# Kernel tuning notes

Hardware: AMD Instinct MI355X
Metric: run time of the kernel (lower is better)

The kernel has to match this reference:

```python
import jax, jax.numpy as jnp
import numpy as np

B, L, D = 16, 96, 512
TAU = 1.0
SLOPE = 0.1  # LeakyReLU negative slope


def setup_inputs() -> dict:
    key = jax.random.key(0)
    k = jax.random.split(key, 6)
    inputs = jax.random.normal(k[0], (B, L, D), dtype=jnp.float32)
    mask = jnp.ones((B, L), dtype=jnp.int32)  # full-length samples
    order = jax.random.randint(k[1], (B, L), 0, L, dtype=jnp.int32)
    # torch Linear default init: U(-1/sqrt(fan_in), 1/sqrt(fan_in))
    s1 = 1.0 / np.sqrt(2 * D)
    s2 = 1.0 / np.sqrt(D)
    W1 = jax.random.uniform(k[2], (2 * D, D), jnp.float32, -s1, s1)
    b1 = jax.random.uniform(k[3], (D,), jnp.float32, -s1, s1)
    W2 = jax.random.uniform(k[4], (D, 1), jnp.float32, -s2, s2)
    b2 = jax.random.uniform(k[5], (1,), jnp.float32, -s2, s2)
    return {"inputs": inputs, "W1": W1, "b1": b1, "W2": W2, "b2": b2,
            "mask": mask, "order": order}


def reference(inputs, W1, b1, W2, b2, mask, order):
    # mask is all-ones -> every sample has length L, so the per-sample
    # slicing in the original is a no-op and we vectorize over the batch.
    # coh[b,i,j] = MLP(concat(x_i, x_j)); split W1 to avoid materializing
    # the [B, L*L, 2D] concatenated feature tensor.
    a = jnp.einsum('bld,dh->blh', inputs, W1[:D])   # contribution of x_i
    c = jnp.einsum('bld,dh->blh', inputs, W1[D:])   # contribution of x_j
    h = a[:, :, None, :] + c[:, None, :, :] + b1    # [B, L, L, D]
    h = jnp.where(h >= 0, h, SLOPE * h)             # LeakyReLU(0.1)
    coh = jnp.einsum('bijh,ho->bij', h, W2) + b2[0]  # [B, L, L]
    logits = coh / TAU

    # gt[b,i,j] = 1 iff order[b,i] - order[b,j] == -1 (j is i's successor)
    diff = order[:, :, None] - order[:, None, :]
    gt = (diff == -1).astype(jnp.int32)
    targets = jnp.argmax(gt, axis=-1).astype(jnp.int32)  # first max, like torch
    last = jnp.argmax(order, axis=-1)                     # last element has no successor
    targets = targets.at[jnp.arange(B), last].set(-1)     # ignore_index

    logp = jax.nn.log_softmax(logits, axis=-1)            # [B, L, L]
    safe_t = jnp.clip(targets, 0)
    picked = jnp.take_along_axis(logp, safe_t[..., None], axis=-1)[..., 0]
    valid = (targets != -1)
    # F.cross_entropy(reduction='mean', ignore_index=-1): mean over valid rows
    per_sample = (jnp.sum(jnp.where(valid, -picked, 0.0), axis=-1)
                  / jnp.sum(valid, axis=-1).astype(logp.dtype))
    return jnp.mean(per_sample)  # sum over samples / B
```

## Files before the change

kernel.cpp:

```cpp
#include <hip/hip_runtime.h>

#define BB 16
#define LL 96
#define DD 512
#define AC_ELEMS (1536 * 512)
#define LOGIT_ELEMS (BB * LL * LL)

__global__ __launch_bounds__(256) void gemm_ac(const float* __restrict__ X,
                                               const float* __restrict__ W1,
                                               const float* __restrict__ b1,
                                               float* __restrict__ a_ws,
                                               float* __restrict__ c_ws) {
  __shared__ float XsT[32][68];
  __shared__ float Ws[32][64];

  const int t = threadIdx.x;
  const int m0 = blockIdx.x * 64;
  const int part = blockIdx.y >> 3;
  const int n0 = (blockIdx.y & 7) * 64;
  const float* __restrict__ Wb = W1 + (size_t)part * (512 * 512);

  float acc[4][4] = {};

  const int r0 = (t >> 4) << 2;
  const int c0 = (t & 15) << 2;
  const int xrow = t >> 3;
  const int xcol = (t & 7) << 2;
  const int wkr = t >> 4;
  const int wc = (t & 15) << 2;

  for (int k0 = 0; k0 < 512; k0 += 32) {
    const float4 xv0 = *(const float4*)(X + (size_t)(m0 + xrow) * 512 + k0 + xcol);
    const float4 xv1 = *(const float4*)(X + (size_t)(m0 + xrow + 32) * 512 + k0 + xcol);
    const float4 wv0 = *(const float4*)(Wb + (size_t)(k0 + wkr) * 512 + n0 + wc);
    const float4 wv1 = *(const float4*)(Wb + (size_t)(k0 + wkr + 16) * 512 + n0 + wc);
    __syncthreads();
    XsT[xcol + 0][xrow] = xv0.x;
    XsT[xcol + 1][xrow] = xv0.y;
    XsT[xcol + 2][xrow] = xv0.z;
    XsT[xcol + 3][xrow] = xv0.w;
    XsT[xcol + 0][xrow + 32] = xv1.x;
    XsT[xcol + 1][xrow + 32] = xv1.y;
    XsT[xcol + 2][xrow + 32] = xv1.z;
    XsT[xcol + 3][xrow + 32] = xv1.w;
    *(float4*)&Ws[wkr][wc] = wv0;
    *(float4*)&Ws[wkr + 16][wc] = wv1;
    __syncthreads();

#pragma unroll
    for (int kk = 0; kk < 32; ++kk) {
      const float4 av = *(const float4*)&XsT[kk][r0];
      const float4 bv = *(const float4*)&Ws[kk][c0];
      acc[0][0] = fmaf(av.x, bv.x, acc[0][0]);
      acc[0][1] = fmaf(av.x, bv.y, acc[0][1]);
      acc[0][2] = fmaf(av.x, bv.z, acc[0][2]);
      acc[0][3] = fmaf(av.x, bv.w, acc[0][3]);
      acc[1][0] = fmaf(av.y, bv.x, acc[1][0]);
      acc[1][1] = fmaf(av.y, bv.y, acc[1][1]);
      acc[1][2] = fmaf(av.y, bv.z, acc[1][2]);
      acc[1][3] = fmaf(av.y, bv.w, acc[1][3]);
      acc[2][0] = fmaf(av.z, bv.x, acc[2][0]);
      acc[2][1] = fmaf(av.z, bv.y, acc[2][1]);
      acc[2][2] = fmaf(av.z, bv.z, acc[2][2]);
      acc[2][3] = fmaf(av.z, bv.w, acc[2][3]);
      acc[3][0] = fmaf(av.w, bv.x, acc[3][0]);
      acc[3][1] = fmaf(av.w, bv.y, acc[3][1]);
      acc[3][2] = fmaf(av.w, bv.z, acc[3][2]);
      acc[3][3] = fmaf(av.w, bv.w, acc[3][3]);
    }
  }

  float* __restrict__ outp = (part == 0) ? a_ws : c_ws;
  float4 bias;
  if (part == 0)
    bias = *(const float4*)(b1 + n0 + c0);
  else
    bias = make_float4(0.f, 0.f, 0.f, 0.f);
#pragma unroll
  for (int ri = 0; ri < 4; ++ri) {
    float4 v;
    v.x = acc[ri][0] + bias.x;
    v.y = acc[ri][1] + bias.y;
    v.z = acc[ri][2] + bias.z;
    v.w = acc[ri][3] + bias.w;
    *(float4*)(outp + (size_t)(m0 + r0 + ri) * 512 + n0 + c0) = v;
  }
}

__global__ __launch_bounds__(256) void coh_kernel(const float* __restrict__ a_ws,
                                                  const float* __restrict__ c_ws,
                                                  const float* __restrict__ W2,
                                                  float* __restrict__ logits) {
  __shared__ float As[16][516];
  __shared__ float Cs[16][516];
  __shared__ float w2s[512];

  const int b = blockIdx.x;
  const int it = blockIdx.y;
  const int jt = blockIdx.z;
  const int t = threadIdx.x;

  const float* __restrict__ abase = a_ws + ((size_t)b * 96 + it * 16) * 512;
  const float* __restrict__ cbase = c_ws + ((size_t)b * 96 + jt * 16) * 512;

#pragma unroll
  for (int p = 0; p < 8; ++p) {
    const int idx = p * 256 + t;
    const int row = idx >> 7;
    const int col = (idx & 127) << 2;
    *(float4*)&As[row][col] = *(const float4*)(abase + (size_t)row * 512 + col);
    *(float4*)&Cs[row][col] = *(const float4*)(cbase + (size_t)row * 512 + col);
  }
  if (t < 128) *(float4*)&w2s[t << 2] = *(const float4*)(W2 + (t << 2));
  __syncthreads();

  const int il = t >> 4;
  const int jl = t & 15;
  float acc = 0.f;
#pragma unroll 8
  for (int h = 0; h < 512; h += 4) {
    const float4 av = *(const float4*)&As[il][h];
    const float4 cv = *(const float4*)&Cs[jl][h];
    const float4 wv = *(const float4*)&w2s[h];
    float x;
    x = av.x + cv.x; acc = fmaf(fmaxf(x, 0.1f * x), wv.x, acc);
    x = av.y + cv.y; acc = fmaf(fmaxf(x, 0.1f * x), wv.y, acc);
    x = av.z + cv.z; acc = fmaf(fmaxf(x, 0.1f * x), wv.z, acc);
    x = av.w + cv.w; acc = fmaf(fmaxf(x, 0.1f * x), wv.w, acc);
  }
  logits[((size_t)b * 96 + it * 16 + il) * 96 + jt * 16 + jl] = acc;
}

__global__ __launch_bounds__(256) void loss_kernel(const float* __restrict__ logits,
                                                   const int* __restrict__ order,
                                                   float* __restrict__ out) {
  __shared__ float wsum[4];
  const int b = blockIdx.x / 6;
  const int rg = (blockIdx.x % 6) * 16;
  const int t = threadIdx.x;
  const int w = t >> 6;
  const int lane = t & 63;

  const int* __restrict__ ob = order + b * 96;
  const int ov = ob[lane];
  const int ov2 = (lane < 32) ? ob[64 + lane] : (int)0x80000000;

  int mo = (ov > ov2) ? ov : ov2;
#pragma unroll
  for (int d = 1; d < 64; d <<= 1) {
    const int o = __shfl_xor(mo, d);
    mo = (o > mo) ? o : mo;
  }
  const unsigned long long lm1 = __ballot(ov == mo);
  const unsigned long long lm2 = __ballot(lane < 32 && ov2 == mo);
  const int last = lm1 ? (__ffsll(lm1) - 1) : (64 + __ffsll(lm2) - 1);

  float lsum = 0.f;
  for (int r = rg + w; r < rg + 16; r += 4) {
    const float* __restrict__ lr = logits + ((size_t)b * 96 + r) * 96;
    const float l1 = lr[lane];
    const float l2 = (lane < 32) ? lr[64 + lane] : -1e30f;
    float m = fmaxf(l1, l2);
#pragma unroll
    for (int d = 1; d < 64; d <<= 1) m = fmaxf(m, __shfl_xor(m, d));
    float s = __expf(l1 - m) + ((lane < 32) ? __expf(l2 - m) : 0.f);
#pragma unroll
    for (int d = 1; d < 64; d <<= 1) s += __shfl_xor(s, d);
    const float lse = m + __logf(s);

    if (r != last) {
      const int oi = ob[r];
      const unsigned long long c1 = __ballot(ov == oi + 1);
      const unsigned long long c2 = __ballot(lane < 32 && ov2 == oi + 1);
      const int tj = c1 ? (__ffsll(c1) - 1) : (c2 ? (64 + __ffsll(c2) - 1) : 0);
      lsum += lse - lr[tj];
    }
  }
  if (lane == 0) wsum[w] = lsum;
  __syncthreads();
  if (t == 0) {
    atomicAdd(out, (wsum[0] + wsum[1] + wsum[2] + wsum[3]) * (1.0f / (16.0f * 95.0f)));
  }
}

extern "C" void kernel_launch(void* const* d_in, const int* in_sizes, int n_in,
                              void* d_out, int out_size, void* d_ws, size_t ws_size,
                              hipStream_t stream) {
  const float* X = (const float*)d_in[0];
  const float* W1 = (const float*)d_in[1];
  const float* b1 = (const float*)d_in[2];
  const float* W2 = (const float*)d_in[3];
  const int* order = (const int*)d_in[6];
  float* out = (float*)d_out;

  float* ws = (float*)d_ws;
  float* a_ws = ws;
  float* c_ws = ws + AC_ELEMS;
  float* logits = ws + 2 * AC_ELEMS;

  hipMemsetAsync(out, 0, sizeof(float), stream);
  gemm_ac<<<dim3(24, 16), 256, 0, stream>>>(X, W1, b1, a_ws, c_ws);
  coh_kernel<<<dim3(16, 6, 6), 256, 0, stream>>>(a_ws, c_ws, W2, logits);
  loss_kernel<<<96, 256, 0, stream>>>(logits, order, out);
}
```

Measured before the change: 121.7 us.

## Use bf16 MFMA for projection GEMM and register-tile the pairwise MLP kernel

Adds a prep kernel that converts X to bf16 and transposes W1 to bf16, then computes the two projection GEMMs with 16x16x32 bf16 MFMA instructions instead of fp32 FMA. The pairwise LeakyReLU/W2 kernel now computes a 2x2 output tile per thread over H chunks staged through shared memory, which cuts LDS traffic per output. This lowers the precision of the GEMM inputs and adds an extra launch plus conversion traffic on every call.

```diff
diff --git a/kernel.cpp b/kernel.cpp
--- a/kernel.cpp
+++ b/kernel.cpp
@@ -3,132 +3,182 @@
 #define BB 16
 #define LL 96
 #define DD 512
-#define AC_ELEMS (1536 * 512)
-#define LOGIT_ELEMS (BB * LL * LL)
-
-__global__ __launch_bounds__(256) void gemm_ac(const float* __restrict__ X,
-                                               const float* __restrict__ W1,
-                                               const float* __restrict__ b1,
-                                               float* __restrict__ a_ws,
-                                               float* __restrict__ c_ws) {
-  __shared__ float XsT[32][68];
-  __shared__ float Ws[32][64];
-
-  const int t = threadIdx.x;
-  const int m0 = blockIdx.x * 64;
-  const int part = blockIdx.y >> 3;
-  const int n0 = (blockIdx.y & 7) * 64;
-  const float* __restrict__ Wb = W1 + (size_t)part * (512 * 512);
-
-  float acc[4][4] = {};
-
-  const int r0 = (t >> 4) << 2;
-  const int c0 = (t & 15) << 2;
-  const int xrow = t >> 3;
-  const int xcol = (t & 7) << 2;
-  const int wkr = t >> 4;
-  const int wc = (t & 15) << 2;
+
+typedef short bf16x8 __attribute__((ext_vector_type(8)));
+typedef float f32x4 __attribute__((ext_vector_type(4)));
+typedef unsigned short us4 __attribute__((ext_vector_type(4)));
+
+static __device__ __forceinline__ unsigned short f2b(float f) {
+  union { float f; unsigned int u; } v; v.f = f;
+  unsigned int r = (v.u + 0x7FFFu + ((v.u >> 16) & 1u)) >> 16;
+  return (unsigned short)r;
+}
+
+__global__ __launch_bounds__(256) void prep(const float* __restrict__ X,
+                                            const float* __restrict__ W1,
+                                            unsigned short* __restrict__ xb,
+                                            unsigned short* __restrict__ w1t) {
+  const int t = threadIdx.x;
+  if (blockIdx.x < 768) {
+    const int g = blockIdx.x * 256 + t;
+    const float4 v = *(const float4*)(X + (size_t)g * 4);
+    us4 o;
+    o[0] = f2b(v.x); o[1] = f2b(v.y); o[2] = f2b(v.z); o[3] = f2b(v.w);
+    *(us4*)(xb + (size_t)g * 4) = o;
+  } else {
+    __shared__ float T[32][36];
+    const int tid = blockIdx.x - 768;
+    const int hb = tid & 15;
+    const int db = tid >> 4;
+    const int r = t >> 3;
+    const int c = (t & 7) * 4;
+    const float4 v = *(const float4*)(W1 + (size_t)(db * 32 + r) * 512 + hb * 32 + c);
+    T[r][c] = v.x; T[r][c + 1] = v.y; T[r][c + 2] = v.z; T[r][c + 3] = v.w;
+    __syncthreads();
+    us4 o;
+    o[0] = f2b(T[c + 0][r]); o[1] = f2b(T[c + 1][r]);
+    o[2] = f2b(T[c + 2][r]); o[3] = f2b(T[c + 3][r]);
+    const size_t idx = (size_t)(db >> 4) * (512 * 512) +
+                       (size_t)(hb * 32 + r) * 512 + (db & 15) * 32 + c;
+    *(us4*)(w1t + idx) = o;
+  }
+}
+
+__global__ __launch_bounds__(128) void gemm_mfma(const unsigned short* __restrict__ xb,
+                                                 const unsigned short* __restrict__ w1t,
+                                                 const float* __restrict__ bvec,
+                                                 float* __restrict__ a_ws,
+                                                 float* __restrict__ c_ws) {
+  __shared__ short Asm[32][40];
+  __shared__ short Bsm[64][40];
+  const int t = threadIdx.x;
+  const int m0 = blockIdx.x * 32;
+  const int n0 = blockIdx.y * 64;
+  const int part = blockIdx.z;
+  const unsigned short* __restrict__ Bg = w1t + (size_t)part * (512 * 512);
+  const int lane = t & 63;
+  const int w = t >> 6;
+
+  f32x4 acc[2][2] = {};
+
+  const int ar = t >> 2;
+  const int akq = (t & 3) << 3;
+  const int fr = lane & 15;
+  const int fg = lane >> 4;
 
   for (int k0 = 0; k0 < 512; k0 += 32) {
-    const float4 xv0 = *(const float4*)(X + (size_t)(m0 + xrow) * 512 + k0 + xcol);
-    const float4 xv1 = *(const float4*)(X + (size_t)(m0 + xrow + 32) * 512 + k0 + xcol);
-    const float4 wv0 = *(const float4*)(Wb + (size_t)(k0 + wkr) * 512 + n0 + wc);
-    const float4 wv1 = *(const float4*)(Wb + (size_t)(k0 + wkr + 16) * 512 + n0 + wc);
-    __syncthreads();
-    XsT[xcol + 0][xrow] = xv0.x;
-    XsT[xcol + 1][xrow] = xv0.y;
-    XsT[xcol + 2][xrow] = xv0.z;
-    XsT[xcol + 3][xrow] = xv0.w;
-    XsT[xcol + 0][xrow + 32] = xv1.x;
-    XsT[xcol + 1][xrow + 32] = xv1.y;
-    XsT[xcol + 2][xrow + 32] = xv1.z;
-    XsT[xcol + 3][xrow + 32] = xv1.w;
-    *(float4*)&Ws[wkr][wc] = wv0;
-    *(float4*)&Ws[wkr + 16][wc] = wv1;
-    __syncthreads();
-
-#pragma unroll
-    for (int kk = 0; kk < 32; ++kk) {
-      const float4 av = *(const float4*)&XsT[kk][r0];
-      const float4 bv = *(const float4*)&Ws[kk][c0];
-      acc[0][0] = fmaf(av.x, bv.x, acc[0][0]);
-      acc[0][1] = fmaf(av.x, bv.y, acc[0][1]);
-      acc[0][2] = fmaf(av.x, bv.z, acc[0][2]);
-      acc[0][3] = fmaf(av.x, bv.w, acc[0][3]);
-      acc[1][0] = fmaf(av.y, bv.x, acc[1][0]);
-      acc[1][1] = fmaf(av.y, bv.y, acc[1][1]);
-      acc[1][2] = fmaf(av.y, bv.z, acc[1][2]);
-      acc[1][3] = fmaf(av.y, bv.w, acc[1][3]);
-      acc[2][0] = fmaf(av.z, bv.x, acc[2][0]);
-      acc[2][1] = fmaf(av.z, bv.y, acc[2][1]);
-      acc[2][2] = fmaf(av.z, bv.z, acc[2][2]);
-      acc[2][3] = fmaf(av.z, bv.w, acc[2][3]);
-      acc[3][0] = fmaf(av.w, bv.x, acc[3][0]);
-      acc[3][1] = fmaf(av.w, bv.y, acc[3][1]);
-      acc[3][2] = fmaf(av.w, bv.z, acc[3][2]);
-      acc[3][3] = fmaf(av.w, bv.w, acc[3][3]);
-    }
+    const bf16x8 aval = *(const bf16x8*)(xb + (size_t)(m0 + ar) * 512 + k0 + akq);
+    const int i2 = t + 128;
+    const bf16x8 bv0 = *(const bf16x8*)(Bg + (size_t)(n0 + (t >> 2)) * 512 + k0 + ((t & 3) << 3));
+    const bf16x8 bv1 = *(const bf16x8*)(Bg + (size_t)(n0 + (i2 >> 2)) * 512 + k0 + ((i2 & 3) << 3));
+    __syncthreads();
+    *(bf16x8*)&Asm[ar][akq] = aval;
+    *(bf16x8*)&Bsm[t >> 2][(t & 3) << 3] = bv0;
+    *(bf16x8*)&Bsm[i2 >> 2][(i2 & 3) << 3] = bv1;
+    __syncthreads();
+    const bf16x8 a0 = *(const bf16x8*)&Asm[fr][fg << 3];
+    const bf16x8 a1 = *(const bf16x8*)&Asm[16 + fr][fg << 3];
+    const bf16x8 b0 = *(const bf16x8*)&Bsm[w * 32 + fr][fg << 3];
+    const bf16x8 b1f = *(const bf16x8*)&Bsm[w * 32 + 16 + fr][fg << 3];
+    acc[0][0] = __builtin_amdgcn_mfma_f32_16x16x32_bf16(a0, b0, acc[0][0], 0, 0, 0);
+    acc[0][1] = __builtin_amdgcn_mfma_f32_16x16x32_bf16(a0, b1f, acc[0][1], 0, 0, 0);
+    acc[1][0] = __builtin_amdgcn_mfma_f32_16x16x32_bf16(a1, b0, acc[1][0], 0, 0, 0);
+    acc[1][1] = __builtin_amdgcn_mfma_f32_16x16x32_bf16(a1, b1f, acc[1][1], 0, 0, 0);
   }
 
   float* __restrict__ outp = (part == 0) ? a_ws : c_ws;
-  float4 bias;
-  if (part == 0)
-    bias = *(const float4*)(b1 + n0 + c0);
-  else
-    bias = make_float4(0.f, 0.f, 0.f, 0.f);
-#pragma unroll
-  for (int ri = 0; ri < 4; ++ri) {
-    float4 v;
-    v.x = acc[ri][0] + bias.x;
-    v.y = acc[ri][1] + bias.y;
-    v.z = acc[ri][2] + bias.z;
-    v.w = acc[ri][3] + bias.w;
-    *(float4*)(outp + (size_t)(m0 + r0 + ri) * 512 + n0 + c0) = v;
-  }
-}
-
-__global__ __launch_bounds__(256) void coh_kernel(const float* __restrict__ a_ws,
-                                                  const float* __restrict__ c_ws,
-                                                  const float* __restrict__ W2,
-                                                  float* __restrict__ logits) {
-  __shared__ float As[16][516];
-  __shared__ float Cs[16][516];
+#pragma unroll
+  for (int fn = 0; fn < 2; ++fn) {
+    const int col = n0 + w * 32 + fn * 16 + fr;
+    const float bias = (part == 0) ? bvec[col] : 0.f;
+#pragma unroll
+    for (int fm = 0; fm < 2; ++fm) {
+#pragma unroll
+      for (int r = 0; r < 4; ++r) {
+        const int row = m0 + fm * 16 + fg * 4 + r;
+        outp[(size_t)row * 512 + col] = acc[fm][fn][r] + bias;
+      }
+    }
+  }
+}
+
+__global__ __launch_bounds__(128) void coh2(const float* __restrict__ a_ws,
+                                            const float* __restrict__ c_ws,
+                                            const float* __restrict__ W2,
+                                            float* __restrict__ logits) {
+  __shared__ float As[32][132];
+  __shared__ float Cs[16][132];
   __shared__ float w2s[512];
-
-  const int b = blockIdx.x;
-  const int it = blockIdx.y;
-  const int jt = blockIdx.z;
-  const int t = threadIdx.x;
-
-  const float* __restrict__ abase = a_ws + ((size_t)b * 96 + it * 16) * 512;
-  const float* __restrict__ cbase = c_ws + ((size_t)b * 96 + jt * 16) * 512;
-
-#pragma unroll
-  for (int p = 0; p < 8; ++p) {
-    const int idx = p * 256 + t;
-    const int row = idx >> 7;
-    const int col = (idx & 127) << 2;
-    *(float4*)&As[row][col] = *(const float4*)(abase + (size_t)row * 512 + col);
-    *(float4*)&Cs[row][col] = *(const float4*)(cbase + (size_t)row * 512 + col);
-  }
-  if (t < 128) *(float4*)&w2s[t << 2] = *(const float4*)(W2 + (t << 2));
-  __syncthreads();
-
-  const int il = t >> 4;
-  const int jl = t & 15;
-  float acc = 0.f;
+  const int b = blockIdx.x, it = blockIdx.y, jt = blockIdx.z;
+  const int t = threadIdx.x;
+  const int i0 = it * 32, j0 = jt * 16;
+  const int il = (t >> 3) * 2;
+  const int jl = (t & 7) * 2;
+
+  *(float4*)&w2s[t * 4] = *(const float4*)(W2 + t * 4);
+
+  float acc00 = 0.f, acc01 = 0.f, acc10 = 0.f, acc11 = 0.f;
+  const float* __restrict__ Ab = a_ws + ((size_t)b * 96 + i0) * 512;
+  const float* __restrict__ Cb = c_ws + ((size_t)b * 96 + j0) * 512;
+
+  for (int hc = 0; hc < 512; hc += 128) {
+    float4 ag[8], cg[4];
+#pragma unroll
+    for (int s = 0; s < 8; ++s) {
+      const int idx = t + 128 * s;
+      ag[s] = *(const float4*)(Ab + (size_t)(idx >> 5) * 512 + hc + (idx & 31) * 4);
+    }
+#pragma unroll
+    for (int s = 0; s < 4; ++s) {
+      const int idx = t + 128 * s;
+      cg[s] = *(const float4*)(Cb + (size_t)(idx >> 5) * 512 + hc + (idx & 31) * 4);
+    }
+    __syncthreads();
+#pragma unroll
+    for (int s = 0; s < 8; ++s) {
+      const int idx = t + 128 * s;
+      *(float4*)&As[idx >> 5][(idx & 31) * 4] = ag[s];
+    }
+#pragma unroll
+    for (int s = 0; s < 4; ++s) {
+      const int idx = t + 128 * s;
+      *(float4*)&Cs[idx >> 5][(idx & 31) * 4] = cg[s];
+    }
+    __syncthreads();
+
 #pragma unroll 8
-  for (int h = 0; h < 512; h += 4) {
-    const float4 av = *(const float4*)&As[il][h];
-    const float4 cv = *(const float4*)&Cs[jl][h];
-    const float4 wv = *(const float4*)&w2s[h];
-    float x;
-    x = av.x + cv.x; acc = fmaf(fmaxf(x, 0.1f * x), wv.x, acc);
-    x = av.y + cv.y; acc = fmaf(fmaxf(x, 0.1f * x), wv.y, acc);
-    x = av.z + cv.z; acc = fmaf(fmaxf(x, 0.1f * x), wv.z, acc);
-    x = av.w + cv.w; acc = fmaf(fmaxf(x, 0.1f * x), wv.w, acc);
-  }
-  logits[((size_t)b * 96 + it * 16 + il) * 96 + jt * 16 + jl] = acc;
+    for (int hh = 0; hh < 128; hh += 4) {
+      const float4 a0 = *(const float4*)&As[il][hh];
+      const float4 a1 = *(const float4*)&As[il + 1][hh];
+      const float4 c0 = *(const float4*)&Cs[jl][hh];
+      const float4 c1 = *(const float4*)&Cs[jl + 1][hh];
+      const float4 wv = *(const float4*)&w2s[hc + hh];
+      float x;
+      x = a0.x + c0.x; acc00 = fmaf(fmaxf(x, 0.1f * x), wv.x, acc00);
+      x = a0.x + c1.x; acc01 = fmaf(fmaxf(x, 0.1f * x), wv.x, acc01);
+      x = a1.x + c0.x; acc10 = fmaf(fmaxf(x, 0.1f * x), wv.x, acc10);
+      x = a1.x + c1.x; acc11 = fmaf(fmaxf(x, 0.1f * x), wv.x, acc11);
+      x = a0.y + c0.y; acc00 = fmaf(fmaxf(x, 0.1f * x), wv.y, acc00);
+      x = a0.y + c1.y; acc01 = fmaf(fmaxf(x, 0.1f * x), wv.y, acc01);
+      x = a1.y + c0.y; acc10 = fmaf(fmaxf(x, 0.1f * x), wv.y, acc10);
+      x = a1.y + c1.y; acc11 = fmaf(fmaxf(x, 0.1f * x), wv.y, acc11);
+      x = a0.z + c0.z; acc00 = fmaf(fmaxf(x, 0.1f * x), wv.z, acc00);
+      x = a0.z + c1.z; acc01 = fmaf(fmaxf(x, 0.1f * x), wv.z, acc01);
+      x = a1.z + c0.z; acc10 = fmaf(fmaxf(x, 0.1f * x), wv.z, acc10);
+      x = a1.z + c1.z; acc11 = fmaf(fmaxf(x, 0.1f * x), wv.z, acc11);
+      x = a0.w + c0.w; acc00 = fmaf(fmaxf(x, 0.1f * x), wv.w, acc00);
+      x = a0.w + c1.w; acc01 = fmaf(fmaxf(x, 0.1f * x), wv.w, acc01);
+      x = a1.w + c0.w; acc10 = fmaf(fmaxf(x, 0.1f * x), wv.w, acc10);
+      x = a1.w + c1.w; acc11 = fmaf(fmaxf(x, 0.1f * x), wv.w, acc11);
+    }
+  }
+
+  float* __restrict__ lp0 = logits + ((size_t)b * 96 + i0 + il) * 96 + j0 + jl;
+  float* __restrict__ lp1 = lp0 + 96;
+  float2 v0; v0.x = acc00; v0.y = acc01;
+  float2 v1; v1.x = acc10; v1.y = acc11;
+  *(float2*)lp0 = v0;
+  *(float2*)lp1 = v1;
 }
 
 __global__ __launch_bounds__(256) void loss_kernel(const float* __restrict__ logits,
@@ -193,13 +243,16 @@
   const int* order = (const int*)d_in[6];
   float* out = (float*)d_out;
 
-  float* ws = (float*)d_ws;
-  float* a_ws = ws;
-  float* c_ws = ws + AC_ELEMS;
-  float* logits = ws + 2 * AC_ELEMS;
+  char* base = (char*)d_ws;
+  float* a_ws = (float*)base;
+  float* c_ws = (float*)(base + 3145728);
+  float* logits = (float*)(base + 2 * 3145728);
+  unsigned short* xb = (unsigned short*)(base + 2 * 3145728 + 589824);
+  unsigned short* w1t = (unsigned short*)(base + 2 * 3145728 + 589824 + 1572864);
 
   hipMemsetAsync(out, 0, sizeof(float), stream);
-  gemm_ac<<<dim3(24, 16), 256, 0, stream>>>(X, W1, b1, a_ws, c_ws);
-  coh_kernel<<<dim3(16, 6, 6), 256, 0, stream>>>(a_ws, c_ws, W2, logits);
+  prep<<<1280, 256, 0, stream>>>(X, W1, xb, w1t);
+  gemm_mfma<<<dim3(48, 8, 2), 128, 0, stream>>>(xb, w1t, b1, a_ws, c_ws);
+  coh2<<<dim3(16, 3, 6), 128, 0, stream>>>(a_ws, c_ws, W2, logits);
   loss_kernel<<<96, 256, 0, stream>>>(logits, order, out);
 }
```

Result: no change. 121.9 us (+0.2%).
